# Kernel tuning notes

Hardware: AMD Instinct MI355X
Metric: run time of the kernel (lower is better)

Reference implementation:

```python
import jax, jax.numpy as jnp
import numpy as np

B, T, S, SYM, FFT = 256, 4, 2, 14, 128   # batch, num_tx, streams_per_tx, ofdm symbols, fft size
NSC, GUARD = 108, 10                      # effective subcarriers, guard offset
L = SYM * NSC                             # 1512, de-mash matrix dimension


def setup_inputs() -> dict:
    key = jax.random.key(0)
    k1, k2, k3, k4 = jax.random.split(key, 4)
    scale = 1.0 / np.sqrt(L).astype(np.float32)  # keep C roughly unitary-scaled
    return {
        "x_real": jax.random.normal(k1, (B, T, S, SYM, FFT), jnp.float32),
        "x_imag": jax.random.normal(k2, (B, T, S, SYM, FFT), jnp.float32),
        "C_real": jax.random.normal(k3, (L, L), jnp.float32) * scale,
        "C_imag": jax.random.normal(k4, (L, L), jnp.float32) * scale,
        "sc_ind": jnp.arange(NSC, dtype=jnp.int32) + GUARD,  # effective subcarrier indices
    }


def reference(x_real, x_imag, C_real, C_imag, sc_ind):
    # Complex RG and de-mash matrix
    x = jax.lax.complex(x_real, x_imag)           # [B,T,S,SYM,FFT] complex64
    C = jax.lax.complex(C_real, C_imag)           # [L,L] complex64

    # gather effective subcarriers along last axis
    y = jnp.take(x, sc_ind, axis=-1)              # [B,T,S,SYM,NSC]
    b, t, s, sym, nsc = y.shape

    # flatten_last_dims(y, 2) and multiply from right by C^H (adjoint=True)
    yf = y.reshape(b, t, s, sym * nsc)            # [B,T,S,L]
    yf = jnp.einsum('btsl,ml->btsm', yf, jnp.conj(C))  # y @ C^H
    y = yf.reshape(b, t, s, sym, nsc)             # [B,T,S,SYM,NSC]

    # scatter back into the full grid (equivalent to the transpose/scatter_nd/transpose chain,
    # since sc_ind is unique and the scatter is along the subcarrier axis)
    out = jnp.zeros(x.shape, x.dtype).at[..., sc_ind].set(y)

    # return real/imag stacked so the output is a single float32 array
    return jnp.stack([out.real, out.imag], axis=0)  # [2,B,T,S,SYM,FFT]
```

## Files before the change

### kernel.cpp

```cpp
#include <hip/hip_runtime.h>
#include <cstdint>
#include <cstddef>


typedef _Float16 half_t;
typedef half_t half8 __attribute__((ext_vector_type(8)));
typedef half_t half4 __attribute__((ext_vector_type(4)));
typedef half_t half2_t __attribute__((ext_vector_type(2)));
typedef float floatx4 __attribute__((ext_vector_type(4)));
typedef float floatv4 __attribute__((ext_vector_type(4)));
typedef float floatv2 __attribute__((ext_vector_type(2)));

#define M_DIM 2048
#define K_DIM 3072
#define L_PAD 1536
#define N2_DIM 1536
#define LDIM 1512
#define NSC 108
#define SYMS 14
#define FFT 128
#define GUARD 10
#define ROWLEN (SYMS * FFT)

#define BM 64
#define BN 64
#define BK 64
#define NITER (L_PAD / BK)

#define PA_BLOCKS 3024
#define PW_BLOCKS 4608
#define PP_BLOCKS 48
#define PG_BLOCKS 2240
#define PREP_BLOCKS (PA_BLOCKS + PW_BLOCKS + PP_BLOCKS + PG_BLOCKS)

typedef __attribute__((address_space(3))) uint32_t lds_u32_t;
typedef const __attribute__((address_space(1))) uint32_t glob_u32_t;

__device__ __forceinline__ void gl2lds16(const void* g, void* l) {
    __builtin_amdgcn_global_load_lds((glob_u32_t*)g, (lds_u32_t*)l, 16, 0, 0);
}

__global__ __launch_bounds__(256) void prep_all(
    const float* __restrict__ xr, const float* __restrict__ xi,
    const float* __restrict__ Cr, const float* __restrict__ Ci,
    const int* __restrict__ sc,
    half_t* __restrict__ A, half_t* __restrict__ W, float* __restrict__ out)
{
    const int b = blockIdx.x;
    const int t = threadIdx.x;

    if (b < PA_BLOCKS) {
        int idx = b * 256 + t;
        int jq = idx % 27;
        int rest = idx / 27;
        int sym = rest % 14;
        int row = rest / 14;
        int s0 = sc[4 * jq];
        const float* xrp = xr + (size_t)row * ROWLEN + sym * FFT + s0;
        const float* xip = xi + (size_t)row * ROWLEN + sym * FFT + s0;
        floatv2 r0 = *(const floatv2*)xrp;
        floatv2 r1 = *(const floatv2*)(xrp + 2);
        floatv2 i0 = *(const floatv2*)xip;
        floatv2 i1 = *(const floatv2*)(xip + 2);
        half4 hr = { (half_t)r0.x, (half_t)r0.y, (half_t)r1.x, (half_t)r1.y };
        half4 hi = { (half_t)i0.x, (half_t)i0.y, (half_t)i1.x, (half_t)i1.y };
        size_t dst = (size_t)row * K_DIM + sym * NSC + 4 * jq;
        *(half4*)(A + dst) = hr;
        *(half4*)(A + dst + L_PAD) = hi;
    } else if (b < PA_BLOCKS + PW_BLOCKS) {
        int idx = (b - PA_BLOCKS) * 256 + t;
        int kq = idx % 768;
        int n = idx / 768;
        int k0 = kq * 4;
        floatv4 f = {0.0f, 0.0f, 0.0f, 0.0f};
        if (n < LDIM) {
            if (k0 < L_PAD) {
                if (k0 < LDIM)
                    f = *(const floatv4*)(Cr + (size_t)n * LDIM + k0);
            } else {
                int l = k0 - L_PAD;
                if (l < LDIM)
                    f = *(const floatv4*)(Ci + (size_t)n * LDIM + l);
            }
        }
        half4 h = { (half_t)f.x, (half_t)f.y, (half_t)f.z, (half_t)f.w };
        *(half4*)(W + (size_t)n * K_DIM + k0) = h;
    } else if (b < PA_BLOCKS + PW_BLOCKS + PP_BLOCKS) {
        int idx = (b - PA_BLOCKS - PW_BLOCKS) * 256 + t;
        int c = idx % 6;
        int row = idx / 6;
        int col = (c < 3) ? (LDIM + c * 8) : (L_PAD + LDIM + (c - 3) * 8);
        half8 z = {};
        *(half8*)(A + (size_t)row * K_DIM + col) = z;
    } else {
        int idx = (b - PA_BLOCKS - PW_BLOCKS - PP_BLOCKS) * 256 + t;
        int h = idx % 10;
        int rest = idx / 10;
        int sym = rest % 14;
        int rowri = rest / 14;
        int c0 = (h < 5) ? (2 * h) : (FFT - GUARD + 2 * (h - 5));
        floatv2 z = {0.0f, 0.0f};
        *(floatv2*)(out + (size_t)rowri * ROWLEN + sym * FFT + c0) = z;
    }
}

__global__ __launch_bounds__(256, 3) void gemm_scatter(
    const half_t* __restrict__ A,
    const half_t* __restrict__ W,
    const int* __restrict__ sc,
    float* __restrict__ out)
{
    __shared__ __align__(16) half_t As[BM * 2 * BK];
    __shared__ __align__(16) half_t Ws[BN * 2 * BK];

    const int t = threadIdx.x;
    const int bn = blockIdx.x;
    const int bm = blockIdx.y;
    const int lane = t & 63;
    const int w = t >> 6;
    const int wm = (w >> 1) * 32;
    const int wn = (w & 1) * 32;

    floatx4 aRR[2][2] = {}, aII[2][2] = {}, aIR[2][2] = {}, aRI[2][2] = {};

    const half_t* gA[4];
    const half_t* gW[4];
    half_t* lA[4];
    half_t* lW[4];
#pragma unroll
    for (int r = 0; r < 4; ++r) {
        int c = r * 256 + t;
        int row = c >> 4, slot = c & 15;
        int g = slot ^ (row & 15);
        int gcol = (g < 8) ? g * 8 : (L_PAD + (g - 8) * 8);
        gA[r] = A + (size_t)(bm * BM + row) * K_DIM + gcol;
        lA[r] = As + c * 8;
        gW[r] = W + (size_t)(bn * BN + row) * K_DIM + gcol;
        lW[r] = Ws + c * 8;
    }

    const int fr = lane & 15;
    const int cr = lane >> 4;

    for (int kb = 0; kb < NITER; ++kb) {
        __syncthreads();
#pragma unroll
        for (int r = 0; r < 4; ++r) gl2lds16(gA[r], lA[r]);
#pragma unroll
        for (int r = 0; r < 4; ++r) gl2lds16(gW[r], lW[r]);
#pragma unroll
        for (int r = 0; r < 4; ++r) { gA[r] += BK; gW[r] += BK; }
        __syncthreads();

#pragma unroll
        for (int ss = 0; ss < 2; ++ss) {
            const int sR = ((ss * 4 + cr) ^ fr) * 8;
            const int sI = ((8 + ss * 4 + cr) ^ fr) * 8;
            half8 yr[2], yi[2], cRf[2], cIf[2];
#pragma unroll
            for (int i = 0; i < 2; ++i) {
                int rb = (wm + i * 16 + fr) * (2 * BK);
                yr[i] = *(const half8*)&As[rb + sR];
                yi[i] = *(const half8*)&As[rb + sI];
            }
#pragma unroll
            for (int j = 0; j < 2; ++j) {
                int rb = (wn + j * 16 + fr) * (2 * BK);
                cRf[j] = *(const half8*)&Ws[rb + sR];
                cIf[j] = *(const half8*)&Ws[rb + sI];
            }
#pragma unroll
            for (int i = 0; i < 2; ++i)
#pragma unroll
                for (int j = 0; j < 2; ++j) {
                    aRR[i][j] = __builtin_amdgcn_mfma_f32_16x16x32_f16(
                        yr[i], cRf[j], aRR[i][j], 0, 0, 0);
                    aII[i][j] = __builtin_amdgcn_mfma_f32_16x16x32_f16(
                        yi[i], cIf[j], aII[i][j], 0, 0, 0);
                    aIR[i][j] = __builtin_amdgcn_mfma_f32_16x16x32_f16(
                        yi[i], cRf[j], aIR[i][j], 0, 0, 0);
                    aRI[i][j] = __builtin_amdgcn_mfma_f32_16x16x32_f16(
                        yr[i], cIf[j], aRI[i][j], 0, 0, 0);
                }
        }
    }

    const int rq = lane >> 4;
#pragma unroll
    for (int j = 0; j < 2; ++j) {
        int n = bn * BN + wn + j * 16 + fr;
        if (n >= LDIM) continue;
        int sym = n / NSC;
        int jj = n - sym * NSC;
        size_t colR = (size_t)sym * FFT + sc[jj];
        size_t colI = (size_t)M_DIM * ROWLEN + colR;
#pragma unroll
        for (int i = 0; i < 2; ++i) {
            int m0 = bm * BM + wm + i * 16 + rq * 4;
#pragma unroll
            for (int r = 0; r < 4; ++r) {
                float vr = aRR[i][j][r] + aII[i][j][r];
                float vi = aIR[i][j][r] - aRI[i][j][r];
                out[colR + (size_t)(m0 + r) * ROWLEN] = vr;
                out[colI + (size_t)(m0 + r) * ROWLEN] = vi;
            }
        }
    }
}

extern "C" void kernel_launch(void* const* d_in, const int* in_sizes, int n_in,
                              void* d_out, int out_size, void* d_ws, size_t ws_size,
                              hipStream_t stream) {
    const float* xr = (const float*)d_in[0];
    const float* xi = (const float*)d_in[1];
    const float* Cr = (const float*)d_in[2];
    const float* Ci = (const float*)d_in[3];
    const int* sc   = (const int*)d_in[4];
    float* out = (float*)d_out;

    half_t* Ah = (half_t*)d_ws;
    half_t* Wh = (half_t*)((char*)d_ws + (size_t)M_DIM * K_DIM * 2);

    prep_all<<<PREP_BLOCKS, 256, 0, stream>>>(
        xr, xi, Cr, Ci, sc, Ah, Wh, out);

    dim3 grid(N2_DIM / BN, M_DIM / BM);
    gemm_scatter<<<grid, 256, 0, stream>>>(Ah, Wh, sc, out);
}
```

Measured before the change: 140.4 us.

## Double-buffer LDS tiles to overlap global loads with MFMA compute

Splits the LDS staging buffers into two halves and prefetches the next K tile into the alternate buffer while the current one is consumed by the MFMA loop. Manual s_waitcnt vmcnt(8) waits only on the older batch of loads, and raw s_barrier calls replace __syncthreads. This hides global-to-LDS latency but doubles LDS use, so occupancy drops from 3 to 2 blocks per CU in the launch bounds. It also relies on the hand-written vmcnt being correct, which is risky given that the compiler may reorder loads.

```diff
diff --git a/kernel.cpp b/kernel.cpp
--- a/kernel.cpp
+++ b/kernel.cpp
@@ -104,14 +104,14 @@
     }
 }
 
-__global__ __launch_bounds__(256, 3) void gemm_scatter(
+__global__ __launch_bounds__(256, 2) void gemm_scatter(
     const half_t* __restrict__ A,
     const half_t* __restrict__ W,
     const int* __restrict__ sc,
     float* __restrict__ out)
 {
-    __shared__ __align__(16) half_t As[BM * 2 * BK];
-    __shared__ __align__(16) half_t Ws[BN * 2 * BK];
+    __shared__ __align__(16) half_t As[2][BM * 2 * BK];
+    __shared__ __align__(16) half_t Ws[2][BN * 2 * BK];
 
     const int t = threadIdx.x;
     const int bn = blockIdx.x;
@@ -125,8 +125,7 @@
 
     const half_t* gA[4];
     const half_t* gW[4];
-    half_t* lA[4];
-    half_t* lW[4];
+    int lOff[4];
 #pragma unroll
     for (int r = 0; r < 4; ++r) {
         int c = r * 256 + t;
@@ -134,23 +133,39 @@
         int g = slot ^ (row & 15);
         int gcol = (g < 8) ? g * 8 : (L_PAD + (g - 8) * 8);
         gA[r] = A + (size_t)(bm * BM + row) * K_DIM + gcol;
-        lA[r] = As + c * 8;
         gW[r] = W + (size_t)(bn * BN + row) * K_DIM + gcol;
-        lW[r] = Ws + c * 8;
+        lOff[r] = c * 8;
     }
 
     const int fr = lane & 15;
     const int cr = lane >> 4;
 
+#pragma unroll
+    for (int r = 0; r < 4; ++r) gl2lds16(gA[r], &As[0][lOff[r]]);
+#pragma unroll
+    for (int r = 0; r < 4; ++r) gl2lds16(gW[r], &Ws[0][lOff[r]]);
+#pragma unroll
+    for (int r = 0; r < 4; ++r) { gA[r] += BK; gW[r] += BK; }
+
     for (int kb = 0; kb < NITER; ++kb) {
-        __syncthreads();
-#pragma unroll
-        for (int r = 0; r < 4; ++r) gl2lds16(gA[r], lA[r]);
-#pragma unroll
-        for (int r = 0; r < 4; ++r) gl2lds16(gW[r], lW[r]);
-#pragma unroll
-        for (int r = 0; r < 4; ++r) { gA[r] += BK; gW[r] += BK; }
-        __syncthreads();
+        const int nb = kb & 1;
+
+        __builtin_amdgcn_s_barrier();
+
+        if (kb < NITER - 1) {
+#pragma unroll
+            for (int r = 0; r < 4; ++r) gl2lds16(gA[r], &As[nb ^ 1][lOff[r]]);
+#pragma unroll
+            for (int r = 0; r < 4; ++r) gl2lds16(gW[r], &Ws[nb ^ 1][lOff[r]]);
+#pragma unroll
+            for (int r = 0; r < 4; ++r) { gA[r] += BK; gW[r] += BK; }
+            asm volatile("s_waitcnt vmcnt(8)" ::: "memory");
+        } else {
+            asm volatile("s_waitcnt vmcnt(0)" ::: "memory");
+        }
+
+        __builtin_amdgcn_s_barrier();
+        __builtin_amdgcn_sched_barrier(0);
 
 #pragma unroll
         for (int ss = 0; ss < 2; ++ss) {
@@ -160,14 +175,14 @@
 #pragma unroll
             for (int i = 0; i < 2; ++i) {
                 int rb = (wm + i * 16 + fr) * (2 * BK);
-                yr[i] = *(const half8*)&As[rb + sR];
-                yi[i] = *(const half8*)&As[rb + sI];
+                yr[i] = *(const half8*)&As[nb][rb + sR];
+                yi[i] = *(const half8*)&As[nb][rb + sI];
             }
 #pragma unroll
             for (int j = 0; j < 2; ++j) {
                 int rb = (wn + j * 16 + fr) * (2 * BK);
-                cRf[j] = *(const half8*)&Ws[rb + sR];
-                cIf[j] = *(const half8*)&Ws[rb + sI];
+                cRf[j] = *(const half8*)&Ws[nb][rb + sR];
+                cIf[j] = *(const half8*)&Ws[nb][rb + sI];
             }
 #pragma unroll
             for (int i = 0; i < 2; ++i)
```

Result: slower. 153.7 us (+9.5%).
